# Optimization experiments

Measured on AMD Instinct MI355X. Metric: run time of the kernel, lower is better.

The kernel has to match this reference:

```python
import jax, jax.numpy as jnp
import numpy as np

S, N, K = 8, 2048, 64          # snapshots, atoms, max neighbors (sum of max_num_neighs)
L = 20.0                        # periodic box length
R_CS, R_C = 6.0, 12.0           # smooth cutoff radii
M2 = 16                         # dim_sub_net


def _mlp(x, params, resnet=False):
    # DenseChainNet: Linear -> relu per layer; resnet skip when dims match or double (DeepMD style)
    for W, b in params:
        y = jax.nn.relu(x @ W + b)
        if resnet and y.shape[-1] == x.shape[-1]:
            y = y + x
        elif resnet and y.shape[-1] == 2 * x.shape[-1]:
            y = y + jnp.concatenate([x, x], axis=-1)
        x = y
    return x


def setup_inputs() -> dict:
    ks = jax.random.split(jax.random.key(0), 14)
    inputs = jax.random.uniform(ks[0], (S, N, 3), jnp.float32) * L
    input_types = jax.random.randint(ks[1], (S, N), 0, 2)
    nl = jax.random.randint(ks[2], (S, N, K), 0, N)
    neigh_list = jnp.where(jax.random.uniform(ks[3], (S, N, K)) < 0.2, -1, nl)  # -1 = padded neighbor

    def w(k, i, o):
        return jax.random.normal(k, (i, o), jnp.float32) / np.float32(np.sqrt(i))

    return {
        'inputs': inputs,
        'input_types': input_types,
        'neigh_list': neigh_list,
        'length': jnp.array([L, L, L], jnp.float32),
        # embed_species (species_dim [2,16,32])
        'ew0': w(ks[4], 2, 16), 'eb0': jnp.zeros((16,), jnp.float32),
        'ew1': w(ks[5], 16, 32), 'eb1': jnp.zeros((32,), jnp.float32),
        # fit_species (species_fit [32,32,31])
        'fw0': w(ks[6], 32, 32), 'fb0': jnp.zeros((32,), jnp.float32),
        'fw1': w(ks[7], 32, 31), 'fb1': jnp.zeros((31,), jnp.float32),
        # embed_net (descript_dim [32,64,128], resnet=True)
        'gw0': w(ks[8], 32, 64), 'gb0': jnp.zeros((64,), jnp.float32),
        'gw1': w(ks[9], 64, 128), 'gb1': jnp.zeros((128,), jnp.float32),
    }


def reference(inputs, input_types, neigh_list, length,
              ew0, eb0, ew1, eb1, fw0, fb0, fw1, fb1, gw0, gb0, gw1, gb1):
    mask = neigh_list == -1                                   # [S,N,K]
    idx = jnp.where(mask, 0, neigh_list)

    # ---- gen_coordinates_smooth: neighbor gather + min-image + smooth cutoff ----
    neigh_pos = jax.vmap(lambda p, i: p[i])(inputs, idx)      # [S,N,K,3]
    diff = neigh_pos - inputs[:, :, None, :]
    diff = diff - length * jnp.round(diff / length)           # minimum image convention
    rsq = jnp.sum(diff * diff, axis=-1)
    r = jnp.sqrt(jnp.where(rsq > 0, rsq, 1.0))                # safe sqrt (self/padded pairs)
    inv = 1.0 / r
    u = (r - R_CS) / (R_C - R_CS)
    sw = jnp.where(r < R_CS, inv,
                   jnp.where(r < R_C, inv * (0.5 * jnp.cos(jnp.pi * u) + 0.5), 0.0))
    valid = (~mask) & (rsq > 0)
    s_ij = jnp.where(valid, sw, 0.0)                          # [S,N,K]  s(r)
    r_ij = diff * (s_ij / r)[..., None]                       # [S,N,K,3] s(r)*x/r

    # ---- SpeciesModule: pair-type embedding (symmetrized) ----
    neigh_types = jax.vmap(lambda t, i: t[i])(input_types, idx)           # [S,N,K]
    center = jnp.broadcast_to(input_types[:, :, None], (S, N, K))
    pairs = jnp.stack([center, neigh_types], axis=-1).astype(jnp.float32).reshape(-1, 2)
    emb = [(ew0, eb0), (ew1, eb1)]
    t = _mlp(pairs, emb) + _mlp(pairs[:, ::-1], emb)
    td = _mlp(t, [(fw0, fb0), (fw1, fb1)]).reshape(S, N, K, -1)           # [S,N,K,31]
    td = jnp.where(mask[..., None], 0.0, td)

    # ---- embedding net + descriptor contraction ----
    s_tilde = jnp.concatenate([td, s_ij[..., None]], axis=-1)             # [S,N,K,32]
    G = _mlp(s_tilde.reshape(S * N * K, -1), [(gw0, gb0), (gw1, gb1)],
             resnet=True).reshape(S, N, K, -1)                            # [S,N,K,128]
    r_tilde = jnp.concatenate([s_ij[..., None], r_ij], axis=-1)           # [S,N,K,4]
    G2 = G[..., :M2]
    R = jnp.einsum('snkd,snkm->sndm', r_tilde, G2)                        # [S,N,4,16]
    R1 = jnp.einsum('snkd,sndm->snkm', r_tilde, R)                        # [S,N,K,16]
    D = jnp.einsum('snke,snkm->snem', G, R1)                              # [S,N,128,16]
    return D
```

## Files before the change

kernel.cpp:

```cpp
#include <hip/hip_runtime.h>
#include <math.h>

#define S_DIM 8
#define N_DIM 2048
#define K_DIM 64
#define APW 4
#define ST_ST 40
#define TQ 144
#define TJ (4 * TQ)
#define H1CH (4 * TJ)

typedef __attribute__((ext_vector_type(8))) short bf16x8;
typedef __attribute__((ext_vector_type(4))) float f32x4;
typedef __attribute__((ext_vector_type(4))) int   i32x4;
typedef __attribute__((ext_vector_type(2))) int   i32x2;

__device__ __forceinline__ unsigned asu(float x) {
    union { float f; unsigned u; } v; v.f = x; return v.u;
}
__device__ __forceinline__ unsigned short f2bf(float x) {
    unsigned u = asu(x);
    return (unsigned short)((u + 0x7FFFu + ((u >> 16) & 1u)) >> 16);
}
__device__ __forceinline__ float lo16f(int d) {
    union { unsigned u; float f; } v; v.u = ((unsigned)d) << 16; return v.f;
}
__device__ __forceinline__ float hi16f(int d) {
    union { unsigned u; float f; } v; v.u = ((unsigned)d) & 0xFFFF0000u; return v.f;
}
__device__ __forceinline__ unsigned rne_pk(float x, float y) {
    unsigned ux = asu(x), uy = asu(y);
    return ((ux + 0x7FFFu + ((ux >> 16) & 1u)) >> 16) |
           ((uy + 0x7FFFu + ((uy >> 16) & 1u)) & 0xFFFF0000u);
}
__device__ __forceinline__ unsigned trn_pk(float x, float y) {
    return (asu(x) >> 16) | (asu(y) & 0xFFFF0000u);
}
__device__ __forceinline__ void lds_fence() {
    asm volatile("s_waitcnt lgkmcnt(0)" ::: "memory");
    __builtin_amdgcn_sched_barrier(0);
}
__device__ __forceinline__ f32x4 mfma_k16(unsigned a0, unsigned a1,
                                          unsigned b0, unsigned b1, f32x4 c) {
    union { i32x4 i; bf16x8 b; } ua, ub;
    ua.i = (i32x4){(int)a0, (int)a1, 0, 0};
    ub.i = (i32x4){(int)b0, (int)b1, 0, 0};
    return __builtin_amdgcn_mfma_f32_16x16x32_bf16(ua.b, ub.b, c, 0, 0, 0);
}

__global__ __launch_bounds__(256) void prep_kernel(
        const float* __restrict__ ew0, const float* __restrict__ eb0,
        const float* __restrict__ ew1, const float* __restrict__ eb1,
        const float* __restrict__ fw0, const float* __restrict__ fb0,
        const float* __restrict__ fw1, const float* __restrict__ fb1,
        const float* __restrict__ gw0, const float* __restrict__ gw1,
        unsigned* __restrict__ td_pk,
        unsigned short* __restrict__ w0t, unsigned short* __restrict__ w1t) {
    __shared__ float l_ew0[32], l_eb0[16], l_ew1[512], l_eb1[32];
    __shared__ float l_fw0[1024], l_fb0[32], l_fw1[992], l_fb1[31];
    __shared__ float l_h[4][2][16];
    __shared__ float l_tv[4][32];
    __shared__ float l_f1[4][32];
    __shared__ float l_td[4][32];

    const int tid = threadIdx.x;
    if (tid < 32) l_ew0[tid] = ew0[tid];
    if (tid < 16) l_eb0[tid] = eb0[tid];
    for (int i = tid; i < 512; i += 256) l_ew1[i] = ew1[i];
    if (tid < 32) l_eb1[tid] = eb1[tid];
    for (int i = tid; i < 1024; i += 256) l_fw0[i] = fw0[i];
    if (tid < 32) l_fb0[tid] = fb0[tid];
    for (int i = tid; i < 992; i += 256) l_fw1[i] = fw1[i];
    if (tid < 31) l_fb1[tid] = fb1[tid];
    __syncthreads();

    if (tid < 128) {
        const int p = tid >> 5, ord = (tid >> 4) & 1, j = tid & 15;
        const float c = (float)(p >> 1), t = (float)(p & 1);
        const float x0 = ord ? t : c;
        const float x1 = ord ? c : t;
        l_h[p][ord][j] = fmaxf(x0 * l_ew0[j] + x1 * l_ew0[16 + j] + l_eb0[j], 0.f);
    }
    __syncthreads();
    if (tid < 128) {
        const int p = tid >> 5, j = tid & 31;
        float acc = 0.f;
#pragma unroll
        for (int ord = 0; ord < 2; ord++) {
            float v = l_eb1[j];
#pragma unroll
            for (int i = 0; i < 16; i++) v += l_h[p][ord][i] * l_ew1[i * 32 + j];
            acc += fmaxf(v, 0.f);
        }
        l_tv[p][j] = acc;
    }
    __syncthreads();
    if (tid < 128) {
        const int p = tid >> 5, j = tid & 31;
        float v = l_fb0[j];
#pragma unroll
        for (int i = 0; i < 32; i++) v += l_tv[p][i] * l_fw0[i * 32 + j];
        l_f1[p][j] = fmaxf(v, 0.f);
    }
    __syncthreads();
    if (tid < 128) {
        const int p = tid >> 5, j = tid & 31;
        if (j < 31) {
            float v = l_fb1[j];
#pragma unroll
            for (int i = 0; i < 32; i++) v += l_f1[p][i] * l_fw1[i * 31 + j];
            l_td[p][j] = fmaxf(v, 0.f);
        } else {
            l_td[p][31] = 0.f;
        }
    }
    __syncthreads();
    if (tid < 64) {
        const int p = tid >> 4, i = tid & 15;
        const unsigned lo = f2bf(l_td[p][2 * i]);
        const unsigned hi = (i == 15) ? 0u : (unsigned)f2bf(l_td[p][2 * i + 1]);
        td_pk[tid] = lo | (hi << 16);
    }

    for (int idx = tid; idx < 2048; idx += 256) {
        const int j = idx >> 5, i = idx & 31;
        w0t[idx] = f2bf(gw0[i * 64 + j]);
    }
    for (int idx = tid; idx < 8192; idx += 256) {
        const int e = idx >> 6, j = idx & 63;
        w1t[idx] = f2bf(gw1[j * 128 + e]);
    }
}

__global__ __launch_bounds__(64, 2) void descr_mfma(
    const float* __restrict__ inputs, const int* __restrict__ input_types,
    const int* __restrict__ neigh_list, const float* __restrict__ length,
    const float* __restrict__ gb0, const float* __restrict__ gb1,
    const unsigned* __restrict__ td_pk, const unsigned short* __restrict__ w0t,
    const unsigned short* __restrict__ w1t, float* __restrict__ out)
{
    __shared__ __align__(16) unsigned short s_st[64 * ST_ST];
    __shared__ __align__(16) char s_h1t[2 * H1CH];
    __shared__ __align__(16) float s_rtT[4 * 68];
    __shared__ unsigned s_tdpk[64];
    float* s_A = (float*)s_st;

    const int lane = threadIdx.x;
    const int l15 = lane & 15;
    const int q = lane >> 4;
    const int abase = blockIdx.x * APW;
    const int sidx = abase >> 11;

    bf16x8 w0f[4];
#pragma unroll
    for (int nt = 0; nt < 4; nt++)
        w0f[nt] = *(const bf16x8*)&w0t[(nt * 16 + l15) * 32 + q * 8];
    bf16x8 w1f[8][2];
#pragma unroll
    for (int et = 0; et < 8; et++) {
        w1f[et][0] = *(const bf16x8*)&w1t[(et * 16 + l15) * 64 + q * 8];
        w1f[et][1] = *(const bf16x8*)&w1t[(et * 16 + l15) * 64 + 32 + q * 8];
    }
    f32x4 b0v[4];
#pragma unroll
    for (int jt = 0; jt < 4; jt++)
        b0v[jt] = *(const f32x4*)&gb0[jt * 16 + q * 4];
    float b1f[8];
#pragma unroll
    for (int et = 0; et < 8; et++) b1f[et] = gb1[et * 16 + l15];
    s_tdpk[lane] = td_pk[lane];
    const float Lx = length[0], Ly = length[1], Lz = length[2];
    const float iLx = 1.f / Lx, iLy = 1.f / Ly, iLz = 1.f / Lz;
    const f32x4 zf = {0.f, 0.f, 0.f, 0.f};

    const unsigned h1u  = (unsigned)(unsigned long long)(const void*)&s_h1t[0];
    const int wroff = (l15 >> 2) * TQ + (l15 & 3) * 32 + q * 8;
    const unsigned troff = h1u + (unsigned)(q * TQ + (l15 >> 2) * 32 + (l15 & 3) * 8);
    const int aoff  = (l15 >> 2) * TQ + (l15 & 3) * 32 + (q & 1) * 16;

    int   cnb  = neigh_list[abase * K_DIM + lane];
    float ccx  = inputs[abase * 3 + 0];
    float ccy  = inputs[abase * 3 + 1];
    float ccz  = inputs[abase * 3 + 2];
    int   cct  = input_types[abase];
    int   cidx0 = cnb < 0 ? 0 : cnb;
    float cpx  = inputs[(sidx * N_DIM + cidx0) * 3 + 0];
    float cpy  = inputs[(sidx * N_DIM + cidx0) * 3 + 1];
    float cpz  = inputs[(sidx * N_DIM + cidx0) * 3 + 2];
    int   cntp = input_types[sidx * N_DIM + cidx0];

    for (int aa = 0; aa < APW; aa++) {
        const int atom = abase + aa;
        const bool pf = (aa + 1 < APW);

        int nnb = 0, nct = 0; float ncx = 0.f, ncy = 0.f, ncz = 0.f;
        if (pf) {
            nnb = neigh_list[(atom + 1) * K_DIM + lane];
            ncx = inputs[(atom + 1) * 3 + 0];
            ncy = inputs[(atom + 1) * 3 + 1];
            ncz = inputs[(atom + 1) * 3 + 2];
            nct = input_types[atom + 1];
        }

        lds_fence();

        {
            const bool msk = cnb < 0;
            float dx = cpx - ccx;
            float dy = cpy - ccy;
            float dz = cpz - ccz;
            dx -= Lx * rintf(dx * iLx);
            dy -= Ly * rintf(dy * iLy);
            dz -= Lz * rintf(dz * iLz);
            const float rsq = dx * dx + dy * dy + dz * dz;
            const float r = sqrtf(rsq > 0.f ? rsq : 1.f);
            const float inv = 1.f / r;
            float sw;
            if (r < 6.f) sw = inv;
            else if (r < 12.f) {
                const float u = (r - 6.f) * (1.f / 6.f);
                sw = inv * (0.5f * __cosf(3.14159265358979323846f * u) + 0.5f);
            } else sw = 0.f;
            const bool valid = (!msk) && (rsq > 0.f);
            const float sij = valid ? sw : 0.f;
            const float f = sij * inv;
            s_rtT[0 * 68 + lane] = sij;
            s_rtT[1 * 68 + lane] = dx * f;
            s_rtT[2 * 68 + lane] = dy * f;
            s_rtT[3 * 68 + lane] = dz * f;

            const unsigned* tdr = &s_tdpk[(cct * 2 + cntp) * 16];
            const unsigned zmask = msk ? 0u : 0xFFFFFFFFu;
            unsigned* strow = (unsigned*)&s_st[lane * ST_ST];
#pragma unroll
            for (int i = 0; i < 15; i++) strow[i] = tdr[i] & zmask;
            strow[15] = (tdr[15] & zmask & 0xFFFFu) | (((unsigned)f2bf(sij)) << 16);
        }
        lds_fence();

        unsigned rtp[4][2];
#pragma unroll
        for (int a = 0; a < 4; a++) {
            const f32x4 rv = *(const f32x4*)&s_rtT[(l15 & 3) * 68 + a * 16 + q * 4];
            rtp[a][0] = rne_pk(rv[0], rv[1]);
            rtp[a][1] = rne_pk(rv[2], rv[3]);
        }

        int nidx = 0, nntp = 0; float npx = 0.f, npy = 0.f, npz = 0.f;
        f32x4 Bj[4] = {zf, zf, zf, zf};
        f32x4 AT[8] = {zf, zf, zf, zf, zf, zf, zf, zf};

#pragma unroll
        for (int mt = 0; mt < 4; mt++) {
            const int cb = (mt & 1) * H1CH;
            const bf16x8 afr = *(const bf16x8*)&s_st[(mt * 16 + l15) * ST_ST + q * 8];
            const i32x2 r0 = *(const i32x2*)&s_st[(mt * 16 + l15) * ST_ST + q * 4];
            const i32x2 r1 = *(const i32x2*)&s_st[(mt * 16 + l15) * ST_ST + 16 + q * 4];

            f32x4 c1[4];
#pragma unroll
            for (int jt = 0; jt < 4; jt++)
                c1[jt] = __builtin_amdgcn_mfma_f32_16x16x32_bf16(w0f[jt], afr, zf, 0, 0, 0);

#pragma unroll
            for (int jt = 0; jt < 4; jt++) {
                const i32x2 rr = (jt & 1) ? r1 : r0;
                const float h0 = fmaxf(c1[jt][0] + b0v[jt][0], 0.f) + lo16f(rr[0]);
                const float h1 = fmaxf(c1[jt][1] + b0v[jt][1], 0.f) + hi16f(rr[0]);
                const float h2 = fmaxf(c1[jt][2] + b0v[jt][2], 0.f) + lo16f(rr[1]);
                const float h3 = fmaxf(c1[jt][3] + b0v[jt][3], 0.f) + hi16f(rr[1]);
                i32x2 pk;
                pk[0] = (int)rne_pk(h0, h1);
                pk[1] = (int)rne_pk(h2, h3);
                *(i32x2*)(s_h1t + cb + wroff + jt * TJ) = pk;
            }
            if (mt == 0 && pf) {
                nidx = nnb < 0 ? 0 : nnb;
                const int nbase = (sidx * N_DIM + nidx) * 3;
                npx = inputs[nbase + 0];
                npy = inputs[nbase + 1];
                npz = inputs[nbase + 2];
                nntp = input_types[sidx * N_DIM + nidx];
            }
            lds_fence();

            i32x2 t0, t1, t2, t3;
            {
                const unsigned ta = troff + (unsigned)cb;
                asm volatile("ds_read_b64_tr_b16 %0, %1" : "=v"(t0) : "v"(ta));
                asm volatile("ds_read_b64_tr_b16 %0, %1" : "=v"(t1) : "v"(ta + TJ));
                asm volatile("ds_read_b64_tr_b16 %0, %1" : "=v"(t2) : "v"(ta + 2 * TJ));
                asm volatile("ds_read_b64_tr_b16 %0, %1" : "=v"(t3) : "v"(ta + 3 * TJ));
            }
            asm volatile("s_waitcnt lgkmcnt(0)" ::: "memory");
            __builtin_amdgcn_sched_barrier(0);
            Bj[0] = mfma_k16(rtp[mt][0], rtp[mt][1], (unsigned)t0[0], (unsigned)t0[1], Bj[0]);
            Bj[1] = mfma_k16(rtp[mt][0], rtp[mt][1], (unsigned)t1[0], (unsigned)t1[1], Bj[1]);
            Bj[2] = mfma_k16(rtp[mt][0], rtp[mt][1], (unsigned)t2[0], (unsigned)t2[1], Bj[2]);
            Bj[3] = mfma_k16(rtp[mt][0], rtp[mt][1], (unsigned)t3[0], (unsigned)t3[1], Bj[3]);

            const bf16x8 a0 = *(const bf16x8*)(s_h1t + cb + aoff + (q >> 1) * TJ);
            const bf16x8 a1 = *(const bf16x8*)(s_h1t + cb + aoff + (2 + (q >> 1)) * TJ);
#pragma unroll
            for (int et = 0; et < 8; et++) {
                f32x4 c2 = __builtin_amdgcn_mfma_f32_16x16x32_bf16(a0, w1f[et][0], zf, 0, 0, 0);
                c2 = __builtin_amdgcn_mfma_f32_16x16x32_bf16(a1, w1f[et][1], c2, 0, 0, 0);
                const float g0 = fmaxf(c2[0] + b1f[et], 0.f);
                const float g1 = fmaxf(c2[1] + b1f[et], 0.f);
                const float g2 = fmaxf(c2[2] + b1f[et], 0.f);
                const float g3 = fmaxf(c2[3] + b1f[et], 0.f);
                AT[et] = mfma_k16(rtp[mt][0], rtp[mt][1],
                                  trn_pk(g0, g1), trn_pk(g2, g3), AT[et]);
            }
        }

        if (lane < 16) {
#pragma unroll
            for (int et = 0; et < 8; et++) {
                const f32x4 v = AT[et] + Bj[et & 3];
                *(f32x4*)&s_A[(et * 16 + lane) * 4] = v;
            }
        }
        lds_fence();

        {
            const int m0 = (lane & 3) * 4;
            const int er = lane >> 2;
            f32x4 Am[4];
#pragma unroll
            for (int t = 0; t < 4; t++) Am[t] = *(const f32x4*)&s_A[(m0 + t) * 4];
            float* op = out + (size_t)atom * 2048;
#pragma unroll
            for (int g = 0; g < 8; g++) {
                const int e = g * 16 + er;
                const f32x4 Ae = *(const f32x4*)&s_A[e * 4];
                f32x4 o;
                o[0] = Ae[0]*Am[0][0] + Ae[1]*Am[0][1] + Ae[2]*Am[0][2] + Ae[3]*Am[0][3];
                o[1] = Ae[0]*Am[1][0] + Ae[1]*Am[1][1] + Ae[2]*Am[1][2] + Ae[3]*Am[1][3];
                o[2] = Ae[0]*Am[2][0] + Ae[1]*Am[2][1] + Ae[2]*Am[2][2] + Ae[3]*Am[2][3];
                o[3] = Ae[0]*Am[3][0] + Ae[1]*Am[3][1] + Ae[2]*Am[3][2] + Ae[3]*Am[3][3];
                *(f32x4*)&op[e * 16 + m0] = o;
            }
        }

        cnb = nnb; ccx = ncx; ccy = ncy; ccz = ncz; cct = nct;
        cpx = npx; cpy = npy; cpz = npz; cntp = nntp;
    }
}

extern "C" void kernel_launch(void* const* d_in, const int* in_sizes, int n_in,
                              void* d_out, int out_size, void* d_ws, size_t ws_size,
                              hipStream_t stream) {
    (void)in_sizes; (void)n_in; (void)out_size; (void)ws_size;
    const float* inputs      = (const float*)d_in[0];
    const int*   input_types = (const int*)d_in[1];
    const int*   neigh_list  = (const int*)d_in[2];
    const float* length      = (const float*)d_in[3];
    const float* ew0 = (const float*)d_in[4];
    const float* eb0 = (const float*)d_in[5];
    const float* ew1 = (const float*)d_in[6];
    const float* eb1 = (const float*)d_in[7];
    const float* fw0 = (const float*)d_in[8];
    const float* fb0 = (const float*)d_in[9];
    const float* fw1 = (const float*)d_in[10];
    const float* fb1 = (const float*)d_in[11];
    const float* gw0 = (const float*)d_in[12];
    const float* gb0 = (const float*)d_in[13];
    const float* gw1 = (const float*)d_in[14];
    const float* gb1 = (const float*)d_in[15];
    float* out = (float*)d_out;

    unsigned* td_pk = (unsigned*)d_ws;
    unsigned short* w0t = (unsigned short*)((char*)d_ws + 512);
    unsigned short* w1t = (unsigned short*)((char*)d_ws + 512 + 4096);

    hipLaunchKernelGGL(prep_kernel, dim3(1), dim3(256), 0, stream,
                       ew0, eb0, ew1, eb1, fw0, fb0, fw1, fb1, gw0, gw1,
                       td_pk, w0t, w1t);

    const int nblocks = (S_DIM * N_DIM) / APW;
    hipLaunchKernelGGL(descr_mfma, dim3(nblocks), dim3(64), 0, stream,
                       inputs, input_types, neigh_list, length,
                       gb0, gb1, td_pk, w0t, w1t, out);
}
```

Baseline: 218.9 us.

## Pack four waves per block and share w1 weights in swizzled LDS

The kernel now runs four waves per block, each with its own LDS slice. The second-layer weight fragments move from per-wave registers into a shared, bank-swizzled LDS copy loaded once per block. The per-neighbor type/s_ij input tile is no longer staged in LDS; it is rebuilt per MFMA tile with ds_bpermute from a packed per-lane word, and the h1 double buffer is dropped. The aim is to free many VGPRs and LDS for higher occupancy, at the cost of extra LDS reads for weights and biases inside the inner loop.

After: 221.6 us. No clear change (+1.2%).

```diff
diff --git a/kernel.cpp b/kernel.cpp
--- a/kernel.cpp
+++ b/kernel.cpp
@@ -5,10 +5,11 @@
 #define N_DIM 2048
 #define K_DIM 64
 #define APW 4
-#define ST_ST 40
+#define WAVES 4
 #define TQ 144
 #define TJ (4 * TQ)
-#define H1CH (4 * TJ)
+#define H1B (4 * TJ)
+#define SLICE 3392
 
 typedef __attribute__((ext_vector_type(8))) short bf16x8;
 typedef __attribute__((ext_vector_type(4))) float f32x4;
@@ -132,51 +133,59 @@
     }
 }
 
-__global__ __launch_bounds__(64, 2) void descr_mfma(
+__global__ __launch_bounds__(256, 3) void descr_mfma(
     const float* __restrict__ inputs, const int* __restrict__ input_types,
     const int* __restrict__ neigh_list, const float* __restrict__ length,
     const float* __restrict__ gb0, const float* __restrict__ gb1,
     const unsigned* __restrict__ td_pk, const unsigned short* __restrict__ w0t,
     const unsigned short* __restrict__ w1t, float* __restrict__ out)
 {
-    __shared__ __align__(16) unsigned short s_st[64 * ST_ST];
-    __shared__ __align__(16) char s_h1t[2 * H1CH];
-    __shared__ __align__(16) float s_rtT[4 * 68];
+    __shared__ __align__(16) char s_pool[WAVES * SLICE];
+    __shared__ __align__(16) char s_w1[16384];
     __shared__ unsigned s_tdpk[64];
-    float* s_A = (float*)s_st;
-
-    const int lane = threadIdx.x;
+    __shared__ float s_gb0f[64];
+
+    const int tid = threadIdx.x;
+    const int lane = tid & 63;
+    const int w = tid >> 6;
     const int l15 = lane & 15;
     const int q = lane >> 4;
-    const int abase = blockIdx.x * APW;
-    const int sidx = abase >> 11;
+
+    if (tid < 64) { s_tdpk[tid] = td_pk[tid]; s_gb0f[tid] = gb0[tid]; }
+    for (int m = tid; m < 1024; m += 256) {
+        const int e = m >> 3, c = m & 7;
+        const i32x4 v = *(const i32x4*)&w1t[e * 64 + c * 8];
+        *(i32x4*)(s_w1 + e * 128 + (((c + e) & 7) << 4)) = v;
+    }
+    __syncthreads();
+
+    char* const slice = s_pool + w * SLICE;
+    float* const s_rt = (float*)slice;
+    char*  const h1t  = slice + 1088;
+    float* const s_A  = (float*)(slice + 1088);
+    const unsigned h1u = (unsigned)(unsigned long long)(const void*)h1t;
+
+    const int wroff = (l15 >> 2) * TQ + (l15 & 3) * 32 + q * 8;
+    const unsigned troff = h1u + (unsigned)(q * TQ + (l15 >> 2) * 32 + (l15 & 3) * 8);
+    const int aoff  = (l15 >> 2) * TQ + (l15 & 3) * 32 + (q & 1) * 16;
+    const char* const w1r = s_w1 + l15 * 128;
+    const int wo0 = ((q + l15) & 7) << 4;
+    const int wo1 = ((q + 4 + l15) & 7) << 4;
 
     bf16x8 w0f[4];
 #pragma unroll
     for (int nt = 0; nt < 4; nt++)
         w0f[nt] = *(const bf16x8*)&w0t[(nt * 16 + l15) * 32 + q * 8];
-    bf16x8 w1f[8][2];
-#pragma unroll
-    for (int et = 0; et < 8; et++) {
-        w1f[et][0] = *(const bf16x8*)&w1t[(et * 16 + l15) * 64 + q * 8];
-        w1f[et][1] = *(const bf16x8*)&w1t[(et * 16 + l15) * 64 + 32 + q * 8];
-    }
-    f32x4 b0v[4];
-#pragma unroll
-    for (int jt = 0; jt < 4; jt++)
-        b0v[jt] = *(const f32x4*)&gb0[jt * 16 + q * 4];
     float b1f[8];
 #pragma unroll
     for (int et = 0; et < 8; et++) b1f[et] = gb1[et * 16 + l15];
-    s_tdpk[lane] = td_pk[lane];
+
     const float Lx = length[0], Ly = length[1], Lz = length[2];
     const float iLx = 1.f / Lx, iLy = 1.f / Ly, iLz = 1.f / Lz;
     const f32x4 zf = {0.f, 0.f, 0.f, 0.f};
 
-    const unsigned h1u  = (unsigned)(unsigned long long)(const void*)&s_h1t[0];
-    const int wroff = (l15 >> 2) * TQ + (l15 & 3) * 32 + q * 8;
-    const unsigned troff = h1u + (unsigned)(q * TQ + (l15 >> 2) * 32 + (l15 & 3) * 8);
-    const int aoff  = (l15 >> 2) * TQ + (l15 & 3) * 32 + (q & 1) * 16;
+    const int abase = (blockIdx.x * WAVES + w) * APW;
+    const int sidx = abase >> 11;
 
     int   cnb  = neigh_list[abase * K_DIM + lane];
     float ccx  = inputs[abase * 3 + 0];
@@ -204,6 +213,7 @@
 
         lds_fence();
 
+        unsigned pinfo;
         {
             const bool msk = cnb < 0;
             float dx = cpx - ccx;
@@ -224,24 +234,19 @@
             const bool valid = (!msk) && (rsq > 0.f);
             const float sij = valid ? sw : 0.f;
             const float f = sij * inv;
-            s_rtT[0 * 68 + lane] = sij;
-            s_rtT[1 * 68 + lane] = dx * f;
-            s_rtT[2 * 68 + lane] = dy * f;
-            s_rtT[3 * 68 + lane] = dz * f;
-
-            const unsigned* tdr = &s_tdpk[(cct * 2 + cntp) * 16];
-            const unsigned zmask = msk ? 0u : 0xFFFFFFFFu;
-            unsigned* strow = (unsigned*)&s_st[lane * ST_ST];
-#pragma unroll
-            for (int i = 0; i < 15; i++) strow[i] = tdr[i] & zmask;
-            strow[15] = (tdr[15] & zmask & 0xFFFFu) | (((unsigned)f2bf(sij)) << 16);
+            s_rt[0 * 68 + lane] = sij;
+            s_rt[1 * 68 + lane] = dx * f;
+            s_rt[2 * 68 + lane] = dy * f;
+            s_rt[3 * 68 + lane] = dz * f;
+            pinfo = ((unsigned)f2bf(sij) << 16) |
+                    (unsigned)((cct << 1) + cntp) | (msk ? 256u : 0u);
         }
         lds_fence();
 
         unsigned rtp[4][2];
 #pragma unroll
         for (int a = 0; a < 4; a++) {
-            const f32x4 rv = *(const f32x4*)&s_rtT[(l15 & 3) * 68 + a * 16 + q * 4];
+            const f32x4 rv = *(const f32x4*)&s_rt[(l15 & 3) * 68 + a * 16 + q * 4];
             rtp[a][0] = rne_pk(rv[0], rv[1]);
             rtp[a][1] = rne_pk(rv[2], rv[3]);
         }
@@ -252,10 +257,29 @@
 
 #pragma unroll
         for (int mt = 0; mt < 4; mt++) {
-            const int cb = (mt & 1) * H1CH;
-            const bf16x8 afr = *(const bf16x8*)&s_st[(mt * 16 + l15) * ST_ST + q * 8];
-            const i32x2 r0 = *(const i32x2*)&s_st[(mt * 16 + l15) * ST_ST + q * 4];
-            const i32x2 r1 = *(const i32x2*)&s_st[(mt * 16 + l15) * ST_ST + 16 + q * 4];
+            const unsigned pk =
+                (unsigned)__builtin_amdgcn_ds_bpermute((mt * 16 + l15) << 2, (int)pinfo);
+            const unsigned pair = pk & 3u;
+            const unsigned zm = (pk & 256u) ? 0u : 0xFFFFFFFFu;
+            const unsigned ksij = pk & 0xFFFF0000u;
+            const unsigned* trow = &s_tdpk[pair * 16];
+            i32x4 tq = *(const i32x4*)&trow[q * 4];
+            i32x2 rd0 = *(const i32x2*)&trow[2 * q];
+            i32x2 rd1 = *(const i32x2*)&trow[8 + 2 * q];
+            tq[0] = (int)((unsigned)tq[0] & zm);
+            tq[1] = (int)((unsigned)tq[1] & zm);
+            tq[2] = (int)((unsigned)tq[2] & zm);
+            tq[3] = (int)((unsigned)tq[3] & zm);
+            rd0[0] = (int)((unsigned)rd0[0] & zm);
+            rd0[1] = (int)((unsigned)rd0[1] & zm);
+            rd1[0] = (int)((unsigned)rd1[0] & zm);
+            rd1[1] = (int)((unsigned)rd1[1] & zm);
+            if (q == 3) {
+                tq[3]  = (int)(((unsigned)tq[3]  & 0xFFFFu) | ksij);
+                rd1[1] = (int)(((unsigned)rd1[1] & 0xFFFFu) | ksij);
+            }
+            union { i32x4 i; bf16x8 b; } ua; ua.i = tq;
+            const bf16x8 afr = ua.b;
 
             f32x4 c1[4];
 #pragma unroll
@@ -264,15 +288,16 @@
 
 #pragma unroll
             for (int jt = 0; jt < 4; jt++) {
-                const i32x2 rr = (jt & 1) ? r1 : r0;
-                const float h0 = fmaxf(c1[jt][0] + b0v[jt][0], 0.f) + lo16f(rr[0]);
-                const float h1 = fmaxf(c1[jt][1] + b0v[jt][1], 0.f) + hi16f(rr[0]);
-                const float h2 = fmaxf(c1[jt][2] + b0v[jt][2], 0.f) + lo16f(rr[1]);
-                const float h3 = fmaxf(c1[jt][3] + b0v[jt][3], 0.f) + hi16f(rr[1]);
-                i32x2 pk;
-                pk[0] = (int)rne_pk(h0, h1);
-                pk[1] = (int)rne_pk(h2, h3);
-                *(i32x2*)(s_h1t + cb + wroff + jt * TJ) = pk;
+                const f32x4 bb = *(const f32x4*)&s_gb0f[jt * 16 + q * 4];
+                const i32x2 rr = (jt & 1) ? rd1 : rd0;
+                const float h0 = fmaxf(c1[jt][0] + bb[0], 0.f) + lo16f(rr[0]);
+                const float h1 = fmaxf(c1[jt][1] + bb[1], 0.f) + hi16f(rr[0]);
+                const float h2 = fmaxf(c1[jt][2] + bb[2], 0.f) + lo16f(rr[1]);
+                const float h3 = fmaxf(c1[jt][3] + bb[3], 0.f) + hi16f(rr[1]);
+                i32x2 pkv;
+                pkv[0] = (int)rne_pk(h0, h1);
+                pkv[1] = (int)rne_pk(h2, h3);
+                *(i32x2*)(h1t + wroff + jt * TJ) = pkv;
             }
             if (mt == 0 && pf) {
                 nidx = nnb < 0 ? 0 : nnb;
@@ -285,13 +310,10 @@
             lds_fence();
 
             i32x2 t0, t1, t2, t3;
-            {
-                const unsigned ta = troff + (unsigned)cb;
-                asm volatile("ds_read_b64_tr_b16 %0, %1" : "=v"(t0) : "v"(ta));
-                asm volatile("ds_read_b64_tr_b16 %0, %1" : "=v"(t1) : "v"(ta + TJ));
-                asm volatile("ds_read_b64_tr_b16 %0, %1" : "=v"(t2) : "v"(ta + 2 * TJ));
-                asm volatile("ds_read_b64_tr_b16 %0, %1" : "=v"(t3) : "v"(ta + 3 * TJ));
-            }
+            asm volatile("ds_read_b64_tr_b16 %0, %1" : "=v"(t0) : "v"(troff));
+            asm volatile("ds_read_b64_tr_b16 %0, %1" : "=v"(t1) : "v"(troff + TJ));
+            asm volatile("ds_read_b64_tr_b16 %0, %1" : "=v"(t2) : "v"(troff + 2 * TJ));
+            asm volatile("ds_read_b64_tr_b16 %0, %1" : "=v"(t3) : "v"(troff + 3 * TJ));
             asm volatile("s_waitcnt lgkmcnt(0)" ::: "memory");
             __builtin_amdgcn_sched_barrier(0);
             Bj[0] = mfma_k16(rtp[mt][0], rtp[mt][1], (unsigned)t0[0], (unsigned)t0[1], Bj[0]);
@@ -299,12 +321,14 @@
             Bj[2] = mfma_k16(rtp[mt][0], rtp[mt][1], (unsigned)t2[0], (unsigned)t2[1], Bj[2]);
             Bj[3] = mfma_k16(rtp[mt][0], rtp[mt][1], (unsigned)t3[0], (unsigned)t3[1], Bj[3]);
 
-            const bf16x8 a0 = *(const bf16x8*)(s_h1t + cb + aoff + (q >> 1) * TJ);
-            const bf16x8 a1 = *(const bf16x8*)(s_h1t + cb + aoff + (2 + (q >> 1)) * TJ);
+            const bf16x8 a0 = *(const bf16x8*)(h1t + aoff + (q >> 1) * TJ);
+            const bf16x8 a1 = *(const bf16x8*)(h1t + aoff + (2 + (q >> 1)) * TJ);
 #pragma unroll
             for (int et = 0; et < 8; et++) {
-                f32x4 c2 = __builtin_amdgcn_mfma_f32_16x16x32_bf16(a0, w1f[et][0], zf, 0, 0, 0);
-                c2 = __builtin_amdgcn_mfma_f32_16x16x32_bf16(a1, w1f[et][1], c2, 0, 0, 0);
+                const bf16x8 wf0 = *(const bf16x8*)(w1r + et * 2048 + wo0);
+                const bf16x8 wf1 = *(const bf16x8*)(w1r + et * 2048 + wo1);
+                f32x4 c2 = __builtin_amdgcn_mfma_f32_16x16x32_bf16(a0, wf0, zf, 0, 0, 0);
+                c2 = __builtin_amdgcn_mfma_f32_16x16x32_bf16(a1, wf1, c2, 0, 0, 0);
                 const float g0 = fmaxf(c2[0] + b1f[et], 0.f);
                 const float g1 = fmaxf(c2[1] + b1f[et], 0.f);
                 const float g2 = fmaxf(c2[2] + b1f[et], 0.f);
@@ -378,8 +402,8 @@
                        ew0, eb0, ew1, eb1, fw0, fb0, fw1, fb1, gw0, gw1,
                        td_pk, w0t, w1t);
 
-    const int nblocks = (S_DIM * N_DIM) / APW;
-    hipLaunchKernelGGL(descr_mfma, dim3(nblocks), dim3(64), 0, stream,
+    const int nblocks = (S_DIM * N_DIM) / (WAVES * APW);
+    hipLaunchKernelGGL(descr_mfma, dim3(nblocks), dim3(256), 0, stream,
                        inputs, input_types, neigh_list, length,
                        gb0, gb1, td_pk, w0t, w1t, out);
 }
```
